# Kernel tuning notes

Hardware: AMD Instinct MI355X
Metric: run time of the kernel (lower is better)

Reference implementation:

```python
import jax, jax.numpy as jnp
import numpy as np

B, D, N, H, K = 8192, 1024, 4096, 8, 4
T, DECAY, STEPS = 100.0, 0.001, 3


def setup_inputs() -> dict:
    key = jax.random.key(0)
    ks = jax.random.split(key, 16)
    rn = lambda k, sh, s=0.02: jax.random.normal(k, sh, jnp.float32) * s
    return {
        'query': jax.random.normal(ks[0], (B, D), jnp.float32),
        'wm': jax.random.normal(ks[1], (B, D), jnp.float32),
        'keys': jax.random.normal(ks[2], (N, D), jnp.float32) * 0.1,
        'values': jax.random.normal(ks[3], (N, D), jnp.float32) * 0.1,
        'last_access': jax.random.uniform(ks[4], (N,), jnp.float32) * T,
        'importance': jnp.ones((N,), jnp.float32),
        'consolid': jnp.ones((N,), jnp.float32),
        'emo_tags': jax.random.uniform(ks[5], (N, 8), jnp.float32),
        'active': jnp.ones((N,), jnp.float32),
        'in_proj_w': rn(ks[6], (3 * D, D)), 'in_proj_b': jnp.zeros((3 * D,), jnp.float32),
        'out_w': rn(ks[7], (D, D)), 'out_b': jnp.zeros((D,), jnp.float32),
        'msg_w1': rn(ks[8], (D, 2 * D)), 'msg_b1': jnp.zeros((D,), jnp.float32),
        'msg_ln_g': jnp.ones((D,), jnp.float32), 'msg_ln_b': jnp.zeros((D,), jnp.float32),
        'msg_w2': rn(ks[9], (D, D)), 'msg_b2': jnp.zeros((D,), jnp.float32),
        'gru_wih': rn(ks[10], (3 * D, D)), 'gru_whh': rn(ks[11], (3 * D, D)),
        'gru_bih': jnp.zeros((3 * D,), jnp.float32), 'gru_bhh': jnp.zeros((3 * D,), jnp.float32),
        'rsn_w1': rn(ks[12], (D, D)), 'rsn_b1': jnp.zeros((D,), jnp.float32),
        'rsn_ln_g': jnp.ones((D,), jnp.float32), 'rsn_ln_b': jnp.zeros((D,), jnp.float32),
        'rsn_w2': rn(ks[13], (D, D)), 'rsn_b2': jnp.zeros((D,), jnp.float32),
        'top_k': K,
    }


def _ln(x, g, b):
    m = x.mean(-1, keepdims=True)
    v = ((x - m) ** 2).mean(-1, keepdims=True)
    return (x - m) / jnp.sqrt(v + 1e-5) * g + b


def reference(query, wm, keys, values, last_access, importance, consolid, emo_tags, active,
              in_proj_w, in_proj_b, out_w, out_b,
              msg_w1, msg_b1, msg_ln_g, msg_ln_b, msg_w2, msg_b2,
              gru_wih, gru_whh, gru_bih, gru_bhh,
              rsn_w1, rsn_b1, rsn_ln_g, rsn_ln_b, rsn_w2, rsn_b2, top_k):
    sg = jax.lax.stop_gradient
    # --- schema retrieve: cosine sim + forgetting-decay + boosts + topk softmax gather ---
    qn = query / jnp.maximum(jnp.linalg.norm(query, axis=-1, keepdims=True), 1e-8)
    kn = keys / jnp.maximum(jnp.linalg.norm(keys, axis=-1, keepdims=True), 1e-8)
    sims = qn @ kn.T  # [B, N]
    forget = sg(jnp.exp(-DECAY * (T - last_access)))
    boost = sg(emo_tags.sum(-1) * 0.1 + importance * 0.2 + jnp.log1p(consolid) * 0.1)
    scores = (sims * forget + boost) * sg(active)
    top_s, top_i = jax.lax.top_k(scores, top_k)  # [B, K]
    w = jax.nn.softmax(top_s, axis=-1)
    schema = jnp.einsum('bk,bkd->bd', w, values[top_i])  # [B, D]

    # --- GraphReasoner: 3 steps of 2-token MHA + msg_net + GRUCell ---
    dh = D // H
    scale = 1.0 / np.sqrt(dh).astype(np.float32)

    def mha(x):  # x [B, 2, D]
        qkv = x @ in_proj_w.T + in_proj_b
        q, k, v = jnp.split(qkv, 3, axis=-1)
        q = q.reshape(-1, 2, H, dh); k = k.reshape(-1, 2, H, dh); v = v.reshape(-1, 2, H, dh)
        a = jax.nn.softmax(jnp.einsum('bqhd,bkhd->bhqk', q, k) * scale, axis=-1)
        o = jnp.einsum('bhqk,bkhd->bqhd', a, v).reshape(-1, 2, D)
        return o @ out_w.T + out_b

    def gru(x, h):
        gi = x @ gru_wih.T + gru_bih
        gh = h @ gru_whh.T + gru_bhh
        ir, iz, inn = jnp.split(gi, 3, axis=-1)
        hr, hz, hn = jnp.split(gh, 3, axis=-1)
        r = jax.nn.sigmoid(ir + hr)
        z = jax.nn.sigmoid(iz + hz)
        n = jnp.tanh(inn + r * hn)
        return (1.0 - z) * n + z * h

    state = wm
    for _ in range(STEPS):
        ctx = jnp.stack([state, schema], axis=1)  # [B, 2, D]
        att = mha(ctx)
        combined = jnp.concatenate([att[:, 0], att[:, 1]], axis=-1)  # [B, 2D]
        msg = jax.nn.relu(_ln(combined @ msg_w1.T + msg_b1, msg_ln_g, msg_ln_b)) @ msg_w2.T + msg_b2
        state = gru(msg, state)
    out = jax.nn.relu(_ln(state @ rsn_w1.T + rsn_b1, rsn_ln_g, rsn_ln_b)) @ rsn_w2.T + rsn_b2
    return out
```

## Files before the change

### kernel.cpp

```cpp
#include <hip/hip_runtime.h>
#include <cstdint>
#include <cstddef>

typedef __attribute__((ext_vector_type(8))) short short8;
typedef __attribute__((ext_vector_type(4))) float f32x4;
typedef __attribute__((ext_vector_type(4))) unsigned short us4;

#define DEVINL static __device__ __forceinline__

DEVINL float bf2f(unsigned short u){
  union { unsigned uu; float f; } v; v.uu = ((unsigned)u) << 16; return v.f;
}
DEVINL unsigned short f2bf(float f){
  unsigned u = __float_as_uint(f);
  u += 0x7fffu + ((u >> 16) & 1u);
  return (unsigned short)(u >> 16);
}

DEVINL bool tk_better(float av, int ai, float bv, int bi){
  return (av > bv) || (av == bv && ai < bi);
}
DEVINL void tk_cmpex(float& va, int& ia, float& vb, int& ib){
  if (!tk_better(va, ia, vb, ib)){
    float tv = va; va = vb; vb = tv;
    int t = ia; ia = ib; ib = t;
  }
}
DEVINL void tk_sort4(float* v, int* id){
  tk_cmpex(v[0], id[0], v[1], id[1]);
  tk_cmpex(v[2], id[2], v[3], id[3]);
  tk_cmpex(v[0], id[0], v[2], id[2]);
  tk_cmpex(v[1], id[1], v[3], id[3]);
  tk_cmpex(v[1], id[1], v[2], id[2]);
}
DEVINL void tk_bmerge(float* v, int* id, const float* pv, const int* pi){
  #pragma unroll
  for (int i = 0; i < 4; ++i){
    bool ta = tk_better(v[i], id[i], pv[3 - i], pi[3 - i]);
    v[i]  = ta ? v[i]  : pv[3 - i];
    id[i] = ta ? id[i] : pi[3 - i];
  }
  tk_cmpex(v[0], id[0], v[2], id[2]);
  tk_cmpex(v[1], id[1], v[3], id[3]);
  tk_cmpex(v[0], id[0], v[1], id[1]);
  tk_cmpex(v[2], id[2], v[3], id[3]);
}

__global__ void k_diag(float* out, float v){ out[0] = v; }

__global__ __launch_bounds__(256) void k_cast_bf16(const float* __restrict__ x,
                                                   unsigned short* __restrict__ y, int n4){
  int stride = gridDim.x * blockDim.x;
  for (int i = blockIdx.x * blockDim.x + threadIdx.x; i < n4; i += stride){
    float4 v = ((const float4*)x)[i];
    us4 o; o[0] = f2bf(v.x); o[1] = f2bf(v.y); o[2] = f2bf(v.z); o[3] = f2bf(v.w);
    ((us4*)y)[i] = o;
  }
}

__global__ __launch_bounds__(256) void k_tcast(const float* __restrict__ in,
    unsigned short* __restrict__ outT, int R, int C){
  __shared__ float t[32][33];
  const int bc = blockIdx.x * 32, br = blockIdx.y * 32;
  const int lx = threadIdx.x & 31, ly = threadIdx.x >> 5;
  #pragma unroll
  for (int i = 0; i < 32; i += 8)
    t[ly + i][lx] = in[(size_t)(br + ly + i) * C + bc + lx];
  __syncthreads();
  #pragma unroll
  for (int i = 0; i < 32; i += 8)
    outT[(size_t)(bc + ly + i) * R + br + lx] = f2bf(t[lx][ly + i]);
}

__global__ __launch_bounds__(256) void k_bias_pre(const float* __restrict__ w1,
    const float* __restrict__ outb, const float* __restrict__ b1, float* __restrict__ bc){
  int wave = threadIdx.x >> 6, lane = threadIdx.x & 63;
  int j = blockIdx.x * 4 + wave;
  float s = 0.f;
  for (int m = lane; m < 2048; m += 64)
    s += w1[(size_t)j * 2048 + m] * outb[m & 1023];
  #pragma unroll
  for (int m = 32; m >= 1; m >>= 1) s += __shfl_xor(s, m);
  if (lane == 0) bc[j] = s + b1[j];
}

__global__ __launch_bounds__(256) void k_bias_gi(const float* __restrict__ wih,
    const float* __restrict__ b2, const float* __restrict__ bih, float* __restrict__ bc){
  int wave = threadIdx.x >> 6, lane = threadIdx.x & 63;
  int n = blockIdx.x * 4 + wave;
  float s = 0.f;
  for (int m = lane; m < 1024; m += 64)
    s += wih[(size_t)n * 1024 + m] * b2[m];
  #pragma unroll
  for (int m = 32; m >= 1; m >>= 1) s += __shfl_xor(s, m);
  if (lane == 0) bc[n] = s + bih[n];
}

__global__ __launch_bounds__(256) void k_prep_keys(const float* __restrict__ keys,
    const float* __restrict__ last_access, const float* __restrict__ importance,
    const float* __restrict__ consolid, const float* __restrict__ emo,
    const float* __restrict__ active, float* __restrict__ ascale, float* __restrict__ bbias){
  int wave = threadIdx.x >> 6, lane = threadIdx.x & 63;
  int n = blockIdx.x * 4 + wave;
  const float* kr = keys + (size_t)n * 1024;
  float s = 0.f;
  #pragma unroll
  for (int j = 0; j < 4; ++j){
    float4 v = ((const float4*)kr)[j * 64 + lane];
    s += v.x*v.x + v.y*v.y + v.z*v.z + v.w*v.w;
  }
  #pragma unroll
  for (int m = 32; m >= 1; m >>= 1) s += __shfl_xor(s, m);
  if (lane == 0){
    float norm = fmaxf(sqrtf(s), 1e-8f);
    float forget = expf(-0.001f * (100.0f - last_access[n]));
    float bo = 0.f;
    #pragma unroll
    for (int j = 0; j < 8; ++j) bo += emo[n * 8 + j];
    bo = bo * 0.1f + importance[n] * 0.2f + log1pf(consolid[n]) * 0.1f;
    float a = active[n];
    ascale[n] = forget * a / norm;
    bbias[n]  = bo * a;
  }
}

__global__ __launch_bounds__(256) void k_qnorm(const float* __restrict__ q, float* __restrict__ qinv){
  int wave = threadIdx.x >> 6, lane = threadIdx.x & 63;
  int b = blockIdx.x * 4 + wave;
  const float* qr = q + (size_t)b * 1024;
  float s = 0.f;
  #pragma unroll
  for (int j = 0; j < 4; ++j){
    float4 v = ((const float4*)qr)[j * 64 + lane];
    s += v.x*v.x + v.y*v.y + v.z*v.z + v.w*v.w;
  }
  #pragma unroll
  for (int m = 32; m >= 1; m >>= 1) s += __shfl_xor(s, m);
  if (lane == 0) qinv[b] = 1.0f / fmaxf(sqrtf(s), 1e-8f);
}

__global__ __launch_bounds__(256) void k_split(const float* __restrict__ X,
    const float* __restrict__ rscale, unsigned short* __restrict__ Hi,
    unsigned short* __restrict__ Lo){
  const int row = blockIdx.x;
  const float sc = rscale ? rscale[row] : 1.0f;
  const int d = threadIdx.x * 4;
  float4 v = *(const float4*)(X + (size_t)row * 1024 + d);
  float xs[4] = {v.x * sc, v.y * sc, v.z * sc, v.w * sc};
  us4 h, l;
  #pragma unroll
  for (int j = 0; j < 4; ++j){
    unsigned short hb = f2bf(xs[j]);
    h[j] = hb;
    l[j] = f2bf(xs[j] - bf2f(hb));
  }
  *(us4*)(Hi + (size_t)row * 1024 + d) = h;
  *(us4*)(Lo + (size_t)row * 1024 + d) = l;
}

__global__ __launch_bounds__(256) void k_scores_mfma(
    const unsigned short* __restrict__ Qhi, const unsigned short* __restrict__ Qlo,
    const unsigned short* __restrict__ Khi, const unsigned short* __restrict__ Klo,
    const float* __restrict__ ascale, const float* __restrict__ bbias,
    float* __restrict__ candV, int* __restrict__ candI){
  __shared__ __align__(16) unsigned short AsH[128 * 32];
  __shared__ __align__(16) unsigned short AsL[128 * 32];
  __shared__ __align__(16) unsigned short BsH[128 * 32];
  __shared__ __align__(16) unsigned short BsL[128 * 32];
  const int tid = threadIdx.x;
  const int wave = tid >> 6, lane = tid & 63;
  const int tM = blockIdx.x, tN = blockIdx.y;
  const int wm_ = wave >> 1, wn_ = wave & 1;
  f32x4 acc[4][4] = {};
  const unsigned short* AH = Qhi + (size_t)tM * 128 * 1024;
  const unsigned short* AL = Qlo + (size_t)tM * 128 * 1024;
  const unsigned short* BH = Khi + (size_t)tN * 128 * 1024;
  const unsigned short* BL = Klo + (size_t)tN * 128 * 1024;
  const int lrow = lane & 15, lk = (lane >> 4) * 8;
  for (int k0 = 0; k0 < 1024; k0 += 32){
    __syncthreads();
    #pragma unroll
    for (int j = 0; j < 2; ++j){
      int c = wave * 128 + j * 64 + lane;
      int row = c >> 2, cp = c & 3;
      size_t go = (size_t)row * 1024 + k0 + cp * 8;
      int lo_ = (wave * 2 + j) * 512;
      __builtin_amdgcn_global_load_lds((const __attribute__((address_space(1))) void*)(AH + go),
          (__attribute__((address_space(3))) void*)(AsH + lo_), 16, 0, 0);
      __builtin_amdgcn_global_load_lds((const __attribute__((address_space(1))) void*)(AL + go),
          (__attribute__((address_space(3))) void*)(AsL + lo_), 16, 0, 0);
      __builtin_amdgcn_global_load_lds((const __attribute__((address_space(1))) void*)(BH + go),
          (__attribute__((address_space(3))) void*)(BsH + lo_), 16, 0, 0);
      __builtin_amdgcn_global_load_lds((const __attribute__((address_space(1))) void*)(BL + go),
          (__attribute__((address_space(3))) void*)(BsL + lo_), 16, 0, 0);
    }
    __syncthreads();
    short8 ah[4], al[4], bh[4], bl[4];
    #pragma unroll
    for (int mi = 0; mi < 4; ++mi){
      int ro = (wm_ * 64 + mi * 16 + lrow) * 32 + lk;
      ah[mi] = *(const short8*)(AsH + ro);
      al[mi] = *(const short8*)(AsL + ro);
    }
    #pragma unroll
    for (int ni = 0; ni < 4; ++ni){
      int ro = (wn_ * 64 + ni * 16 + lrow) * 32 + lk;
      bh[ni] = *(const short8*)(BsH + ro);
      bl[ni] = *(const short8*)(BsL + ro);
    }
    #pragma unroll
    for (int mi = 0; mi < 4; ++mi)
      #pragma unroll
      for (int ni = 0; ni < 4; ++ni){
        acc[mi][ni] = __builtin_amdgcn_mfma_f32_16x16x32_bf16(ah[mi], bh[ni], acc[mi][ni], 0, 0, 0);
        acc[mi][ni] = __builtin_amdgcn_mfma_f32_16x16x32_bf16(ah[mi], bl[ni], acc[mi][ni], 0, 0, 0);
        acc[mi][ni] = __builtin_amdgcn_mfma_f32_16x16x32_bf16(al[mi], bh[ni], acc[mi][ni], 0, 0, 0);
      }
  }
  const int lc = lane & 15;
  float as_[4], bb_[4]; int cid[4];
  #pragma unroll
  for (int ni = 0; ni < 4; ++ni){
    cid[ni] = tN * 128 + wn_ * 64 + ni * 16 + lc;
    as_[ni] = ascale[cid[ni]];
    bb_[ni] = bbias[cid[ni]];
  }
  #pragma unroll
  for (int mi = 0; mi < 4; ++mi){
    #pragma unroll
    for (int r = 0; r < 4; ++r){
      float v[4]; int id[4];
      #pragma unroll
      for (int ni = 0; ni < 4; ++ni){
        v[ni]  = acc[mi][ni][r] * as_[ni] + bb_[ni];
        id[ni] = cid[ni];
      }
      tk_sort4(v, id);
      #pragma unroll
      for (int mask = 1; mask <= 8; mask <<= 1){
        float pv[4]; int pi_[4];
        #pragma unroll
        for (int j = 0; j < 4; ++j){
          pv[j]  = __shfl_xor(v[j], mask);
          pi_[j] = __shfl_xor(id[j], mask);
        }
        tk_bmerge(v, id, pv, pi_);
      }
      if (lc == 0){
        int row = tM * 128 + wm_ * 64 + mi * 16 + (lane >> 4) * 4 + r;
        size_t cb = (size_t)row * 256 + tN * 8 + wn_ * 4;
        #pragma unroll
        for (int j = 0; j < 4; ++j){ candV[cb + j] = v[j]; candI[cb + j] = id[j]; }
      }
    }
  }
}

__global__ __launch_bounds__(256) void k_topk_merge(const float* __restrict__ candV,
    const int* __restrict__ candI, const float* __restrict__ V,
    unsigned short* __restrict__ schema_bf){
  const int row = blockIdx.x, tid = threadIdx.x;
  const int wave = tid >> 6, lane = tid & 63;
  float v[4]; int id[4];
  v[0] = candV[(size_t)row * 256 + tid];
  id[0] = candI[(size_t)row * 256 + tid];
  #pragma unroll
  for (int j = 1; j < 4; ++j){ v[j] = -3.4e38f; id[j] = 0x7fffffff; }
  #pragma unroll
  for (int mask = 1; mask <= 32; mask <<= 1){
    float pv[4]; int pi_[4];
    #pragma unroll
    for (int j = 0; j < 4; ++j){
      pv[j]  = __shfl_xor(v[j], mask);
      pi_[j] = __shfl_xor(id[j], mask);
    }
    tk_bmerge(v, id, pv, pi_);
  }
  __shared__ float wv[4][4]; __shared__ int wi[4][4];
  if (lane == 0){
    #pragma unroll
    for (int j = 0; j < 4; ++j){ wv[wave][j] = v[j]; wi[wave][j] = id[j]; }
  }
  __syncthreads();
  __shared__ float w_sh[4]; __shared__ int i_sh[4];
  if (tid == 0){
    float fv[4]; int fi[4];
    #pragma unroll
    for (int j = 0; j < 4; ++j){ fv[j] = wv[0][j]; fi[j] = wi[0][j]; }
    #pragma unroll
    for (int w = 1; w < 4; ++w){
      float pv[4]; int pi_[4];
      #pragma unroll
      for (int j = 0; j < 4; ++j){ pv[j] = wv[w][j]; pi_[j] = wi[w][j]; }
      tk_bmerge(fv, fi, pv, pi_);
    }
    float m = fv[0];
    float e0 = expf(fv[0] - m), e1 = expf(fv[1] - m), e2 = expf(fv[2] - m), e3 = expf(fv[3] - m);
    float inv = 1.f / (e0 + e1 + e2 + e3);
    w_sh[0] = e0 * inv; w_sh[1] = e1 * inv; w_sh[2] = e2 * inv; w_sh[3] = e3 * inv;
    i_sh[0] = fi[0]; i_sh[1] = fi[1]; i_sh[2] = fi[2]; i_sh[3] = fi[3];
  }
  __syncthreads();
  float w0 = w_sh[0], w1 = w_sh[1], w2 = w_sh[2], w3 = w_sh[3];
  const float* v0 = V + (size_t)i_sh[0] * 1024;
  const float* v1 = V + (size_t)i_sh[1] * 1024;
  const float* v2 = V + (size_t)i_sh[2] * 1024;
  const float* v3 = V + (size_t)i_sh[3] * 1024;
  int d = tid * 4;
  float4 a = *(const float4*)(v0 + d);
  float4 b4 = *(const float4*)(v1 + d);
  float4 c = *(const float4*)(v2 + d);
  float4 e = *(const float4*)(v3 + d);
  us4 o;
  o[0] = f2bf(w0*a.x + w1*b4.x + w2*c.x + w3*e.x);
  o[1] = f2bf(w0*a.y + w1*b4.y + w2*c.y + w3*e.y);
  o[2] = f2bf(w0*a.z + w1*b4.z + w2*c.z + w3*e.z);
  o[3] = f2bf(w0*a.w + w1*b4.w + w2*c.w + w3*e.w);
  *(us4*)(schema_bf + (size_t)row * 1024 + d) = o;
}

__global__ __launch_bounds__(256) void k_initstate(const float* __restrict__ wm,
    float* __restrict__ st, unsigned short* __restrict__ stbf){
  size_t i = ((size_t)blockIdx.x * 256 + threadIdx.x) * 4;
  float4 v = *(const float4*)(wm + i);
  *(float4*)(st + i) = v;
  us4 o; o[0] = f2bf(v.x); o[1] = f2bf(v.y); o[2] = f2bf(v.z); o[3] = f2bf(v.w);
  *(us4*)(stbf + i) = o;
}

template<int OUT_BF16>
__global__ __launch_bounds__(256) void k_gemm(const unsigned short* __restrict__ A,
    const unsigned short* __restrict__ W, const float* __restrict__ bias,
    void* __restrict__ C, int M, int N, int K, int lda, int ldc){
  __shared__ __align__(16) unsigned short As[128 * 32];
  __shared__ __align__(16) unsigned short Ws[128 * 32];
  const int tid = threadIdx.x;
  const int wave = tid >> 6, lane = tid & 63;
  const int tM = blockIdx.x, tN = blockIdx.y;
  const int wm_ = wave >> 1, wn_ = wave & 1;
  f32x4 acc[4][4] = {};
  const unsigned short* Abase = A + (size_t)tM * 128 * lda;
  const unsigned short* Wbase = W + (size_t)tN * 128 * K;
  const int lrow = lane & 15, lk = (lane >> 4) * 8;
  for (int k0 = 0; k0 < K; k0 += 32){
    __syncthreads();
    #pragma unroll
    for (int j = 0; j < 2; ++j){
      int c = wave * 128 + j * 64 + lane;
      int row = c >> 2, cp = c & 3;
      const unsigned short* ga = Abase + (size_t)row * lda + k0 + cp * 8;
      const unsigned short* gw = Wbase + (size_t)row * K + k0 + cp * 8;
      __builtin_amdgcn_global_load_lds((const __attribute__((address_space(1))) void*)ga,
          (__attribute__((address_space(3))) void*)(As + (wave * 2 + j) * 512), 16, 0, 0);
      __builtin_amdgcn_global_load_lds((const __attribute__((address_space(1))) void*)gw,
          (__attribute__((address_space(3))) void*)(Ws + (wave * 2 + j) * 512), 16, 0, 0);
    }
    __syncthreads();
    short8 af[4], bfr[4];
    #pragma unroll
    for (int mi = 0; mi < 4; ++mi)
      af[mi] = *(const short8*)(As + (wm_ * 64 + mi * 16 + lrow) * 32 + lk);
    #pragma unroll
    for (int ni = 0; ni < 4; ++ni)
      bfr[ni] = *(const short8*)(Ws + (wn_ * 64 + ni * 16 + lrow) * 32 + lk);
    #pragma unroll
    for (int mi = 0; mi < 4; ++mi)
      #pragma unroll
      for (int ni = 0; ni < 4; ++ni)
        acc[mi][ni] = __builtin_amdgcn_mfma_f32_16x16x32_bf16(af[mi], bfr[ni], acc[mi][ni], 0, 0, 0);
  }
  const int lc = lane & 15, lr = (lane >> 4) * 4;
  #pragma unroll
  for (int ni = 0; ni < 4; ++ni){
    int col = tN * 128 + wn_ * 64 + ni * 16 + lc;
    float bb = bias ? bias[col] : 0.f;
    #pragma unroll
    for (int mi = 0; mi < 4; ++mi){
      int rowb = tM * 128 + wm_ * 64 + mi * 16 + lr;
      #pragma unroll
      for (int r = 0; r < 4; ++r){
        float vv = acc[mi][ni][r] + bb;
        size_t off = (size_t)(rowb + r) * ldc + col;
        if (OUT_BF16) ((unsigned short*)C)[off] = f2bf(vv);
        else ((float*)C)[off] = vv;
      }
    }
  }
}

__global__ __launch_bounds__(256) void k_attn(const unsigned short* __restrict__ qkvS,
    const unsigned short* __restrict__ qkvM, unsigned short* __restrict__ catt){
  const int b = blockIdx.x, tid = threadIdx.x;
  const int l = tid & 31;
  const int e = (tid >> 5) * 128 + l * 4;
  const unsigned short* ps = qkvS + (size_t)b * 3072;
  const unsigned short* pm = qkvM + (size_t)b * 3072;
  float q0[4], kk0[4], v0[4], q1[4], kk1[4], v1[4];
  us4 t;
  t = *(const us4*)(ps + e);        for (int j = 0; j < 4; ++j) q0[j]  = bf2f(t[j]);
  t = *(const us4*)(ps + 1024 + e); for (int j = 0; j < 4; ++j) kk0[j] = bf2f(t[j]);
  t = *(const us4*)(ps + 2048 + e); for (int j = 0; j < 4; ++j) v0[j]  = bf2f(t[j]);
  t = *(const us4*)(pm + e);        for (int j = 0; j < 4; ++j) q1[j]  = bf2f(t[j]);
  t = *(const us4*)(pm + 1024 + e); for (int j = 0; j < 4; ++j) kk1[j] = bf2f(t[j]);
  t = *(const us4*)(pm + 2048 + e); for (int j = 0; j < 4; ++j) v1[j]  = bf2f(t[j]);
  float s00 = 0.f, s01 = 0.f, s10 = 0.f, s11 = 0.f;
  #pragma unroll
  for (int j = 0; j < 4; ++j){
    s00 += q0[j] * kk0[j]; s01 += q0[j] * kk1[j];
    s10 += q1[j] * kk0[j]; s11 += q1[j] * kk1[j];
  }
  #pragma unroll
  for (int m = 16; m >= 1; m >>= 1){
    s00 += __shfl_xor(s00, m); s01 += __shfl_xor(s01, m);
    s10 += __shfl_xor(s10, m); s11 += __shfl_xor(s11, m);
  }
  const float sc = 0.08838834764831845f;
  s00 *= sc; s01 *= sc; s10 *= sc; s11 *= sc;
  float m0 = fmaxf(s00, s01), m1 = fmaxf(s10, s11);
  float e00 = expf(s00 - m0), e01 = expf(s01 - m0);
  float e10 = expf(s10 - m1), e11 = expf(s11 - m1);
  float i0 = 1.f / (e00 + e01), i1 = 1.f / (e10 + e11);
  float w00 = e00 * i0, w01 = e01 * i0, w10 = e10 * i1, w11 = e11 * i1;
  us4 o0, o1;
  #pragma unroll
  for (int j = 0; j < 4; ++j){
    o0[j] = f2bf(w00 * v0[j] + w01 * v1[j]);
    o1[j] = f2bf(w10 * v0[j] + w11 * v1[j]);
  }
  *(us4*)(catt + (size_t)b * 2048 + e)        = o0;
  *(us4*)(catt + (size_t)b * 2048 + 1024 + e) = o1;
}

__global__ __launch_bounds__(256) void k_ln_relu(const float* __restrict__ X,
    const float* __restrict__ g, const float* __restrict__ bta, unsigned short* __restrict__ Y){
  const int row = blockIdx.x, tid = threadIdx.x;
  const float* x = X + (size_t)row * 1024;
  const int d = tid * 4;
  float4 v = *(const float4*)(x + d);
  float s1 = v.x + v.y + v.z + v.w;
  float s2 = v.x*v.x + v.y*v.y + v.z*v.z + v.w*v.w;
  #pragma unroll
  for (int m = 32; m >= 1; m >>= 1){ s1 += __shfl_xor(s1, m); s2 += __shfl_xor(s2, m); }
  __shared__ float a1[4], a2[4];
  int wave = tid >> 6, lane = tid & 63;
  if (lane == 0){ a1[wave] = s1; a2[wave] = s2; }
  __syncthreads();
  s1 = a1[0] + a1[1] + a1[2] + a1[3];
  s2 = a2[0] + a2[1] + a2[2] + a2[3];
  float mean = s1 * (1.f / 1024.f);
  float var  = s2 * (1.f / 1024.f) - mean * mean;
  float rstd = rsqrtf(var + 1e-5f);
  float4 gg = *(const float4*)(g + d);
  float4 bb = *(const float4*)(bta + d);
  us4 o;
  o[0] = f2bf(fmaxf((v.x - mean) * rstd * gg.x + bb.x, 0.f));
  o[1] = f2bf(fmaxf((v.y - mean) * rstd * gg.y + bb.y, 0.f));
  o[2] = f2bf(fmaxf((v.z - mean) * rstd * gg.z + bb.z, 0.f));
  o[3] = f2bf(fmaxf((v.w - mean) * rstd * gg.w + bb.w, 0.f));
  *(us4*)(Y + (size_t)row * 1024 + d) = o;
}

__global__ __launch_bounds__(256) void k_gru(const unsigned short* __restrict__ gi,
    const unsigned short* __restrict__ gh, const float* __restrict__ h,
    float* __restrict__ hn, unsigned short* __restrict__ hnbf){
  const int b = blockIdx.x;
  const int d = threadIdx.x * 4;
  const unsigned short* pi = gi + (size_t)b * 3072;
  const unsigned short* ph = gh + (size_t)b * 3072;
  us4 t;
  float ir[4], iz[4], in_[4], hr[4], hz[4], hnn[4];
  t = *(const us4*)(pi + d);        for (int j = 0; j < 4; ++j) ir[j]  = bf2f(t[j]);
  t = *(const us4*)(pi + 1024 + d); for (int j = 0; j < 4; ++j) iz[j]  = bf2f(t[j]);
  t = *(const us4*)(pi + 2048 + d); for (int j = 0; j < 4; ++j) in_[j] = bf2f(t[j]);
  t = *(const us4*)(ph + d);        for (int j = 0; j < 4; ++j) hr[j]  = bf2f(t[j]);
  t = *(const us4*)(ph + 1024 + d); for (int j = 0; j < 4; ++j) hz[j]  = bf2f(t[j]);
  t = *(const us4*)(ph + 2048 + d); for (int j = 0; j < 4; ++j) hnn[j] = bf2f(t[j]);
  float4 hv = *(const float4*)(h + (size_t)b * 1024 + d);
  float hvv[4] = {hv.x, hv.y, hv.z, hv.w};
  float ov[4]; us4 ob;
  #pragma unroll
  for (int j = 0; j < 4; ++j){
    float r = 1.f / (1.f + expf(-(ir[j] + hr[j])));
    float z = 1.f / (1.f + expf(-(iz[j] + hz[j])));
    float n = tanhf(in_[j] + r * hnn[j]);
    float o = (1.f - z) * n + z * hvv[j];
    ov[j] = o; ob[j] = f2bf(o);
  }
  float4 of; of.x = ov[0]; of.y = ov[1]; of.z = ov[2]; of.w = ov[3];
  *(float4*)(hn + (size_t)b * 1024 + d) = of;
  *(us4*)(hnbf + (size_t)b * 1024 + d) = ob;
}

extern "C" void kernel_launch(void* const* d_in, const int* in_sizes, int n_in,
                              void* d_out, int out_size, void* d_ws, size_t ws_size,
                              hipStream_t stream) {
  (void)in_sizes; (void)n_in; (void)out_size;
  const float* query       = (const float*)d_in[0];
  const float* wm          = (const float*)d_in[1];
  const float* keys        = (const float*)d_in[2];
  const float* values      = (const float*)d_in[3];
  const float* last_access = (const float*)d_in[4];
  const float* importance  = (const float*)d_in[5];
  const float* consolid    = (const float*)d_in[6];
  const float* emo         = (const float*)d_in[7];
  const float* active      = (const float*)d_in[8];
  const float* in_proj_w   = (const float*)d_in[9];
  const float* in_proj_b   = (const float*)d_in[10];
  const float* out_w       = (const float*)d_in[11];
  const float* out_b       = (const float*)d_in[12];
  const float* msg_w1      = (const float*)d_in[13];
  const float* msg_b1      = (const float*)d_in[14];
  const float* msg_ln_g    = (const float*)d_in[15];
  const float* msg_ln_b    = (const float*)d_in[16];
  const float* msg_w2      = (const float*)d_in[17];
  const float* msg_b2      = (const float*)d_in[18];
  const float* gru_wih     = (const float*)d_in[19];
  const float* gru_whh     = (const float*)d_in[20];
  const float* gru_bih     = (const float*)d_in[21];
  const float* gru_bhh     = (const float*)d_in[22];
  const float* rsn_w1      = (const float*)d_in[23];
  const float* rsn_b1      = (const float*)d_in[24];
  const float* rsn_ln_g    = (const float*)d_in[25];
  const float* rsn_ln_b    = (const float*)d_in[26];
  const float* rsn_w2      = (const float*)d_in[27];
  const float* rsn_b2      = (const float*)d_in[28];
  float* out = (float*)d_out;

  size_t off = 0;
  char* base = (char*)d_ws;
  auto carve = [&](size_t bytes) -> char* {
    char* p = base + off;
    off += (bytes + 255) & ~(size_t)255;
    return p;
  };
  float* ascale = (float*)carve(4096*4);
  float* bbias  = (float*)carve(4096*4);
  float* qinv   = (float*)carve(8192*4);
  float* bc_pre = (float*)carve(1024*4);
  float* bc_gi  = (float*)carve(3072*4);
  unsigned short* wb_inproj = (unsigned short*)carve((size_t)3072*1024*2);
  unsigned short* wb_gwhh   = (unsigned short*)carve((size_t)3072*1024*2);
  unsigned short* wb_rw1    = (unsigned short*)carve((size_t)1024*1024*2);
  unsigned short* wb_rw2    = (unsigned short*)carve((size_t)1024*1024*2);
  unsigned short* wb_Wab    = (unsigned short*)carve((size_t)1024*2048*2);
  unsigned short* wb_Wc     = (unsigned short*)carve((size_t)3072*1024*2);
  unsigned short* schema_bf = (unsigned short*)carve((size_t)8192*1024*2);
  float*          state_f   = (float*)carve((size_t)8192*1024*4);
  unsigned short* state_bf  = (unsigned short*)carve((size_t)8192*1024*2);
  unsigned short* qkvM      = (unsigned short*)carve((size_t)8192*3072*2);
  unsigned short* bufP      = (unsigned short*)carve((size_t)8192*3072*2);
  unsigned short* bufQ      = (unsigned short*)carve((size_t)8192*3072*2);

  if (off > ws_size){
    k_diag<<<1, 1, 0, stream>>>(out, (float)(ws_size >> 20));
    return;
  }

  unsigned short* tmp_w1bf  = bufQ;
  unsigned short* tmp_outwT = bufQ + (size_t)1024*2048;
  unsigned short* tmp_w2T   = tmp_outwT + (size_t)1024*1024;
  unsigned short* tmp_wihbf = tmp_w2T + (size_t)1024*1024;

  unsigned short* Qhi = qkvM;
  unsigned short* Qlo = Qhi + (size_t)8192*1024;
  unsigned short* Khi = Qlo + (size_t)8192*1024;
  unsigned short* Klo = Khi + (size_t)4096*1024;
  float* candV = (float*)bufP;
  int*   candI = (int*)((char*)bufP + (size_t)8192*256*4);

  unsigned short* qkvS  = bufP;
  unsigned short* catt  = bufQ;
  float*          preln = (float*)bufP;
  unsigned short* h1buf = bufQ;
  unsigned short* gibuf = bufP;
  unsigned short* ghbuf = bufQ;

  auto cast = [&](const float* src, unsigned short* dst, int n){
    k_cast_bf16<<<1024, 256, 0, stream>>>(src, dst, n / 4);
  };
  cast(in_proj_w, wb_inproj, 3072*1024);
  cast(gru_whh,   wb_gwhh,   3072*1024);
  cast(rsn_w1,    wb_rw1,    1024*1024);
  cast(rsn_w2,    wb_rw2,    1024*1024);
  cast(msg_w1,    tmp_w1bf,  1024*2048);
  cast(gru_wih,   tmp_wihbf, 3072*1024);
  k_tcast<<<dim3(32, 32), 256, 0, stream>>>(out_w,  tmp_outwT, 1024, 1024);
  k_tcast<<<dim3(32, 32), 256, 0, stream>>>(msg_w2, tmp_w2T,   1024, 1024);
  k_bias_pre<<<256, 256, 0, stream>>>(msg_w1, out_b, msg_b1, bc_pre);
  k_bias_gi<<<768, 256, 0, stream>>>(gru_wih, msg_b2, gru_bih, bc_gi);
  k_gemm<1><<<dim3(8, 8), 256, 0, stream>>>(tmp_w1bf,        tmp_outwT, nullptr, wb_Wab,        1024, 1024, 1024, 2048, 2048);
  k_gemm<1><<<dim3(8, 8), 256, 0, stream>>>(tmp_w1bf + 1024, tmp_outwT, nullptr, wb_Wab + 1024, 1024, 1024, 1024, 2048, 2048);
  k_gemm<1><<<dim3(24, 8), 256, 0, stream>>>(tmp_wihbf, tmp_w2T, nullptr, wb_Wc, 3072, 1024, 1024, 1024, 1024);

  k_qnorm<<<2048, 256, 0, stream>>>(query, qinv);
  k_prep_keys<<<1024, 256, 0, stream>>>(keys, last_access, importance, consolid, emo, active, ascale, bbias);
  k_split<<<8192, 256, 0, stream>>>(query, qinv, Qhi, Qlo);
  k_split<<<4096, 256, 0, stream>>>(keys, nullptr, Khi, Klo);
  k_scores_mfma<<<dim3(64, 32), 256, 0, stream>>>(Qhi, Qlo, Khi, Klo, ascale, bbias, candV, candI);
  k_topk_merge<<<8192, 256, 0, stream>>>(candV, candI, values, schema_bf);

  k_initstate<<<8192, 256, 0, stream>>>(wm, state_f, state_bf);
  k_gemm<1><<<dim3(64, 24), 256, 0, stream>>>(schema_bf, wb_inproj, in_proj_b, qkvM, 8192, 3072, 1024, 1024, 3072);
  for (int s = 0; s < 3; ++s){
    k_gemm<1><<<dim3(64, 24), 256, 0, stream>>>(state_bf, wb_inproj, in_proj_b, qkvS, 8192, 3072, 1024, 1024, 3072);
    k_attn<<<8192, 256, 0, stream>>>(qkvS, qkvM, catt);
    k_gemm<0><<<dim3(64, 8), 256, 0, stream>>>(catt, wb_Wab, bc_pre, preln, 8192, 1024, 2048, 2048, 1024);
    k_ln_relu<<<8192, 256, 0, stream>>>(preln, msg_ln_g, msg_ln_b, h1buf);
    k_gemm<1><<<dim3(64, 24), 256, 0, stream>>>(h1buf, wb_Wc, bc_gi, gibuf, 8192, 3072, 1024, 1024, 3072);
    k_gemm<1><<<dim3(64, 24), 256, 0, stream>>>(state_bf, wb_gwhh, gru_bhh, ghbuf, 8192, 3072, 1024, 1024, 3072);
    k_gru<<<8192, 256, 0, stream>>>(gibuf, ghbuf, state_f, state_f, state_bf);
  }
  k_gemm<0><<<dim3(64, 8), 256, 0, stream>>>(state_bf, wb_rw1, rsn_b1, (float*)bufP, 8192, 1024, 1024, 1024, 1024);
  k_ln_relu<<<8192, 256, 0, stream>>>((float*)bufP, rsn_ln_g, rsn_ln_b, bufQ);
  k_gemm<0><<<dim3(64, 8), 256, 0, stream>>>(bufQ, wb_rw2, rsn_b2, out, 8192, 1024, 1024, 1024, 1024);
}
```

Before: 1.647 ms.

## Add double-buffered 256x256 swizzled-LDS GEMM for the N=3072 projections

Adds a new GEMM kernel with 256x256 output tiles and 512 threads. It double-buffers 64-wide K slices in LDS using direct global-to-LDS loads and an XOR chunk swizzle to avoid bank conflicts. It also remaps workgroups so neighbouring blocks share tiles, and raises wave priority around the MFMA bursts. The in_proj, GRU input and GRU hidden GEMMs now use it, aiming for more data reuse per tile and for load latency hidden behind compute. In exchange it needs 128KB of LDS per block, so only one block fits per CU, and the 384-block grid fills the CUs unevenly, leaving a partial last wave.

```diff
diff --git a/kernel.cpp b/kernel.cpp
--- a/kernel.cpp
+++ b/kernel.cpp
@@ -7,6 +7,8 @@
 typedef __attribute__((ext_vector_type(4))) unsigned short us4;
 
 #define DEVINL static __device__ __forceinline__
+#define AS1 __attribute__((address_space(1)))
+#define AS3 __attribute__((address_space(3)))
 
 DEVINL float bf2f(unsigned short u){
   union { unsigned uu; float f; } v; v.uu = ((unsigned)u) << 16; return v.f;
@@ -185,14 +187,10 @@
       int row = c >> 2, cp = c & 3;
       size_t go = (size_t)row * 1024 + k0 + cp * 8;
       int lo_ = (wave * 2 + j) * 512;
-      __builtin_amdgcn_global_load_lds((const __attribute__((address_space(1))) void*)(AH + go),
-          (__attribute__((address_space(3))) void*)(AsH + lo_), 16, 0, 0);
-      __builtin_amdgcn_global_load_lds((const __attribute__((address_space(1))) void*)(AL + go),
-          (__attribute__((address_space(3))) void*)(AsL + lo_), 16, 0, 0);
-      __builtin_amdgcn_global_load_lds((const __attribute__((address_space(1))) void*)(BH + go),
-          (__attribute__((address_space(3))) void*)(BsH + lo_), 16, 0, 0);
-      __builtin_amdgcn_global_load_lds((const __attribute__((address_space(1))) void*)(BL + go),
-          (__attribute__((address_space(3))) void*)(BsL + lo_), 16, 0, 0);
+      __builtin_amdgcn_global_load_lds((const AS1 void*)(AH + go), (AS3 void*)(AsH + lo_), 16, 0, 0);
+      __builtin_amdgcn_global_load_lds((const AS1 void*)(AL + go), (AS3 void*)(AsL + lo_), 16, 0, 0);
+      __builtin_amdgcn_global_load_lds((const AS1 void*)(BH + go), (AS3 void*)(BsH + lo_), 16, 0, 0);
+      __builtin_amdgcn_global_load_lds((const AS1 void*)(BL + go), (AS3 void*)(BsL + lo_), 16, 0, 0);
     }
     __syncthreads();
     short8 ah[4], al[4], bh[4], bl[4];
@@ -350,10 +348,8 @@
       int row = c >> 2, cp = c & 3;
       const unsigned short* ga = Abase + (size_t)row * lda + k0 + cp * 8;
       const unsigned short* gw = Wbase + (size_t)row * K + k0 + cp * 8;
-      __builtin_amdgcn_global_load_lds((const __attribute__((address_space(1))) void*)ga,
-          (__attribute__((address_space(3))) void*)(As + (wave * 2 + j) * 512), 16, 0, 0);
-      __builtin_amdgcn_global_load_lds((const __attribute__((address_space(1))) void*)gw,
-          (__attribute__((address_space(3))) void*)(Ws + (wave * 2 + j) * 512), 16, 0, 0);
+      __builtin_amdgcn_global_load_lds((const AS1 void*)ga, (AS3 void*)(As + (wave * 2 + j) * 512), 16, 0, 0);
+      __builtin_amdgcn_global_load_lds((const AS1 void*)gw, (AS3 void*)(Ws + (wave * 2 + j) * 512), 16, 0, 0);
     }
     __syncthreads();
     short8 af[4], bfr[4];
@@ -380,6 +376,108 @@
       #pragma unroll
       for (int r = 0; r < 4; ++r){
         float vv = acc[mi][ni][r] + bb;
+        size_t off = (size_t)(rowb + r) * ldc + col;
+        if (OUT_BF16) ((unsigned short*)C)[off] = f2bf(vv);
+        else ((float*)C)[off] = vv;
+      }
+    }
+  }
+}
+
+DEVINL int chunk_swz(int q){ return (q & ~7) | ((q & 7) ^ ((q >> 3) & 7)); }
+
+template<int OUT_BF16>
+__global__ __launch_bounds__(512, 2) void k_gemm256(const unsigned short* __restrict__ A,
+    const unsigned short* __restrict__ W, const float* __restrict__ bias,
+    void* __restrict__ C, int M, int N, int K, int lda, int ldc){
+  __shared__ __align__(16) unsigned short lds[65536];
+  const int tid = threadIdx.x;
+  const int wave = tid >> 6, lane = tid & 63;
+  const int wr = wave >> 2, wc = wave & 3;
+  const int lrow = lane & 15, lkk = lane >> 4;
+
+  const int nwg = gridDim.x * gridDim.y;
+  int lin = blockIdx.y * gridDim.x + blockIdx.x;
+  int cpx = nwg >> 3;
+  int swz = (lin & 7) * cpx + (lin >> 3);
+  const int nM = M >> 8;
+  const int tM = swz % nM, tN = swz / nM;
+
+  const unsigned short* Abase = A + (size_t)tM * 256 * lda;
+  const unsigned short* Wbase = W + (size_t)tN * 256 * K;
+
+  f32x4 acc[8][4] = {};
+
+  auto STAGE = [&](int kt, int buf){
+    const int k0 = kt * 64;
+    #pragma unroll
+    for (int j = 0; j < 4; ++j){
+      int qst = j * 512 + tid;
+      int g = chunk_swz(qst);
+      int row = g >> 3, c = g & 7;
+      int dst = buf * 32768 + (j * 512 + wave * 64) * 8;
+      __builtin_amdgcn_global_load_lds((const AS1 void*)(Abase + (size_t)row * lda + k0 + c * 8),
+          (AS3 void*)(lds + dst), 16, 0, 0);
+      __builtin_amdgcn_global_load_lds((const AS1 void*)(Wbase + (size_t)row * K + k0 + c * 8),
+          (AS3 void*)(lds + 16384 + dst), 16, 0, 0);
+    }
+  };
+
+  const int ntiles = K >> 6;
+  STAGE(0, 0);
+  __syncthreads();
+
+  for (int t = 0; t < ntiles; ++t){
+    const int cur = t & 1;
+    if (t + 1 < ntiles) STAGE(t + 1, cur ^ 1);
+    const int ab = cur * 32768, bb = cur * 32768 + 16384;
+    #pragma unroll
+    for (int mh = 0; mh < 2; ++mh){
+      short8 af[4][2];
+      #pragma unroll
+      for (int mi = 0; mi < 4; ++mi)
+        #pragma unroll
+        for (int kk = 0; kk < 2; ++kk){
+          int q = (wr * 128 + (mh * 4 + mi) * 16 + lrow) * 8 + kk * 4 + lkk;
+          af[mi][kk] = *(const short8*)(lds + ab + chunk_swz(q) * 8);
+        }
+      #pragma unroll
+      for (int nh = 0; nh < 2; ++nh){
+        short8 bf[2][2];
+        #pragma unroll
+        for (int ni = 0; ni < 2; ++ni)
+          #pragma unroll
+          for (int kk = 0; kk < 2; ++kk){
+            int q = (wc * 64 + (nh * 2 + ni) * 16 + lrow) * 8 + kk * 4 + lkk;
+            bf[ni][kk] = *(const short8*)(lds + bb + chunk_swz(q) * 8);
+          }
+        __builtin_amdgcn_s_setprio(1);
+        #pragma unroll
+        for (int mi = 0; mi < 4; ++mi)
+          #pragma unroll
+          for (int ni = 0; ni < 2; ++ni)
+            #pragma unroll
+            for (int kk = 0; kk < 2; ++kk)
+              acc[mh * 4 + mi][nh * 2 + ni] =
+                __builtin_amdgcn_mfma_f32_16x16x32_bf16(af[mi][kk], bf[ni][kk],
+                                                        acc[mh * 4 + mi][nh * 2 + ni], 0, 0, 0);
+        __builtin_amdgcn_s_setprio(0);
+      }
+    }
+    __syncthreads();
+  }
+
+  const int lc = lane & 15, lr = (lane >> 4) * 4;
+  #pragma unroll
+  for (int ni = 0; ni < 4; ++ni){
+    int col = tN * 256 + wc * 64 + ni * 16 + lc;
+    float bb2 = bias ? bias[col] : 0.f;
+    #pragma unroll
+    for (int mi = 0; mi < 8; ++mi){
+      int rowb = tM * 256 + wr * 128 + mi * 16 + lr;
+      #pragma unroll
+      for (int r = 0; r < 4; ++r){
+        float vv = acc[mi][ni][r] + bb2;
         size_t off = (size_t)(rowb + r) * ldc + col;
         if (OUT_BF16) ((unsigned short*)C)[off] = f2bf(vv);
         else ((float*)C)[off] = vv;
@@ -600,14 +698,14 @@
   k_topk_merge<<<8192, 256, 0, stream>>>(candV, candI, values, schema_bf);
 
   k_initstate<<<8192, 256, 0, stream>>>(wm, state_f, state_bf);
-  k_gemm<1><<<dim3(64, 24), 256, 0, stream>>>(schema_bf, wb_inproj, in_proj_b, qkvM, 8192, 3072, 1024, 1024, 3072);
+  k_gemm256<1><<<dim3(32, 12), 512, 0, stream>>>(schema_bf, wb_inproj, in_proj_b, qkvM, 8192, 3072, 1024, 1024, 3072);
   for (int s = 0; s < 3; ++s){
-    k_gemm<1><<<dim3(64, 24), 256, 0, stream>>>(state_bf, wb_inproj, in_proj_b, qkvS, 8192, 3072, 1024, 1024, 3072);
+    k_gemm256<1><<<dim3(32, 12), 512, 0, stream>>>(state_bf, wb_inproj, in_proj_b, qkvS, 8192, 3072, 1024, 1024, 3072);
     k_attn<<<8192, 256, 0, stream>>>(qkvS, qkvM, catt);
     k_gemm<0><<<dim3(64, 8), 256, 0, stream>>>(catt, wb_Wab, bc_pre, preln, 8192, 1024, 2048, 2048, 1024);
     k_ln_relu<<<8192, 256, 0, stream>>>(preln, msg_ln_g, msg_ln_b, h1buf);
-    k_gemm<1><<<dim3(64, 24), 256, 0, stream>>>(h1buf, wb_Wc, bc_gi, gibuf, 8192, 3072, 1024, 1024, 3072);
-    k_gemm<1><<<dim3(64, 24), 256, 0, stream>>>(state_bf, wb_gwhh, gru_bhh, ghbuf, 8192, 3072, 1024, 1024, 3072);
+    k_gemm256<1><<<dim3(32, 12), 512, 0, stream>>>(h1buf, wb_Wc, bc_gi, gibuf, 8192, 3072, 1024, 1024, 3072);
+    k_gemm256<1><<<dim3(32, 12), 512, 0, stream>>>(state_bf, wb_gwhh, gru_bhh, ghbuf, 8192, 3072, 1024, 1024, 3072);
     k_gru<<<8192, 256, 0, stream>>>(gibuf, ghbuf, state_f, state_f, state_bf);
   }
   k_gemm<0><<<dim3(64, 8), 256, 0, stream>>>(state_bf, wb_rw1, rsn_b1, (float*)bufP, 8192, 1024, 1024, 1024, 1024);
```

After: 1.634 ms. About the same (-0.8%).
